# Optimization experiments

Measured on AMD Instinct MI355X. Metric: run time of the kernel, lower is better.

The kernel has to match this reference:

```python
import jax, jax.numpy as jnp
import numpy as np

B, C, H, W = 8, 4, 384, 384


def setup_inputs() -> dict:
    key = jax.random.key(0)
    k1, k2 = jax.random.split(key)
    outputs = jax.random.normal(k1, (B, C, H, W), dtype=jnp.float32)
    targets = jax.random.randint(k2, (B, H, W), 0, C)  # every class present w.h.p.
    return {"outputs": outputs, "targets": targets}


def _edt(is_zero):
    """Exact 2D Euclidean distance transform, batched.

    is_zero: bool [B,C,H,W], True at 'feature' pixels (distance 0 there).
    Returns float32 [B,C,H,W] distance to nearest True pixel.
    Separable exact algorithm (Meijster/Felzenszwalb-Huttenlocher style):
      phase 1: 1D distance along H via forward+backward scans;
      phase 2: dt^2(x,y) = min_j g(x,j)^2 + (y-j)^2 via a scan over y.
    """
    b, c, h, w = is_zero.shape
    BIG = jnp.float32(h + w)  # finite sentinel (exceeds any true distance)

    def pass1(carry, z):
        d = jnp.where(z, jnp.float32(0.0), jnp.minimum(carry + 1.0, BIG))
        return d, d

    init = jnp.full((b, c, w), BIG, jnp.float32)
    zt = jnp.moveaxis(is_zero, 2, 0)  # [H,B,C,W]
    _, fwd = jax.lax.scan(pass1, init, zt)
    _, bwd = jax.lax.scan(pass1, init, zt[::-1])
    g = jnp.minimum(fwd, bwd[::-1])          # [H,B,C,W] vertical 1D distances
    g2 = jnp.moveaxis(g * g, 0, 2)           # [B,C,H,W]

    j = jnp.arange(w, dtype=jnp.float32)     # candidate columns

    def pass2(_, y):
        # min over j of g(x,j)^2 + (y-j)^2  -> [B,C,H]
        return 0, jnp.min(g2 + (y - j) ** 2, axis=-1)

    _, dt2 = jax.lax.scan(pass2, 0, j)       # [W,B,C,H]
    return jnp.sqrt(jnp.moveaxis(dt2, 0, 3))  # [B,C,H,W]


def reference(outputs, targets):
    num_classes = outputs.shape[1]
    # one-hot: true_hot[b,c,h,w] = (targets[b,h,w] == c)
    true_hot = targets[:, None, :, :] == jnp.arange(num_classes)[None, :, None, None]
    dt = _edt(true_hot)                                  # 0 at class pixels
    dmax = jnp.max(dt, axis=(2, 3), keepdims=True)       # per (b,c) slice max
    dist_map = jnp.where(true_hot, -dmax, dt)            # factor = -1
    # weight=None -> ones(C); weight_matrix/weight.sum() == 1/C
    loss = jax.nn.softmax(outputs, axis=1) * dist_map / jnp.float32(num_classes)
    return jnp.mean(loss)
```

## Files before the change

kernel.cpp:

```cpp
#include <hip/hip_runtime.h>

#define B 8
#define C 4
#define H 384
#define W 384
#define HW (H * W)
#define CHW (C * H * W)
#define NTOT (B * CHW)
#define BIG2 589824
#define TPI 144
#define NBLK (B * TPI)
#define PSTR 12
#define LOG2E 1.44269504088896340736f

__device__ __forceinline__ int nearest2(unsigned long long m, int lx, int shl) {
    unsigned long long right = m >> lx;
    int dR = right ? (int)__builtin_ctzll(right) : 999;
    unsigned long long leftb = m << shl;
    int dL = leftb ? (int)__builtin_clzll(leftb) : 999;
    int d = min(dR, dL);
    return d * d;
}

__device__ __attribute__((noinline))
int ring_fallback(const int* __restrict__ tg, int xa, int ya, int c, int best) {
    for (int d = 17; d * d < best; ++d) {
        int xlo = xa - d, xhi = xa + d, ylo = ya - d, yhi = ya + d;
        for (int xx = max(xlo, 0); xx <= min(xhi, W - 1); ++xx) {
            int ddx = xx - xa;
            int bb = ddx * ddx + d * d;
            if (bb < best) {
                if (ylo >= 0 && tg[ylo * W + xx] == c) best = bb;
                if (yhi < H && tg[yhi * W + xx] == c) best = min(best, bb);
            }
        }
        for (int yy = max(ylo + 1, 0); yy <= min(yhi - 1, H - 1); ++yy) {
            int ddy = yy - ya;
            int bb = ddy * ddy + d * d;
            if (bb < best) {
                if (xlo >= 0 && tg[yy * W + xlo] == c) best = bb;
                if (xhi < W && tg[yy * W + xhi] == c) best = min(best, bb);
            }
        }
    }
    return best;
}

__global__ __launch_bounds__(256)
void dist_loss_kernel(const float* __restrict__ outputs,
                      const int* __restrict__ targets,
                      float* __restrict__ parts) {
    __shared__ unsigned long long rowsm[64][4];
    __shared__ unsigned long long big[32 * 18];
    __shared__ float sred[4][9];

    int bid = blockIdx.x;
    int bx = bid % 12, by = (bid / 12) % 12, b = bid / TPI;
    int x0 = bx * 32, y0 = by * 32;
    int tid = threadIdx.x, lane = tid & 63, wv = tid >> 6;
    const int* tg = targets + b * HW;

    bool edge = (bx == 0) | (bx == 11) | (by == 0) | (by == 11);
    if (!edge) {
        const int* tp = tg + (y0 - 16 + wv) * W + (x0 - 16 + lane);
        for (int i = 0; i < 16; ++i) {
            int r = i * 4 + wv;
            int tv = tp[i * 4 * W];
            unsigned long long m0 = __ballot(tv == 0);
            unsigned long long m1 = __ballot(tv == 1);
            unsigned long long m2 = __ballot(tv == 2);
            unsigned long long m3 = __ballot(tv == 3);
            if (lane == 0) {
                rowsm[r][0] = m0; rowsm[r][1] = m1;
                rowsm[r][2] = m2; rowsm[r][3] = m3;
            }
        }
    } else {
        for (int i = 0; i < 16; ++i) {
            int r = i * 4 + wv;
            int ya = y0 - 16 + r, xa = x0 - 16 + lane;
            bool valid = (ya >= 0) & (ya < H) & (xa >= 0) & (xa < W);
            int yc = min(max(ya, 0), H - 1), xc = min(max(xa, 0), W - 1);
            int tv = tg[yc * W + xc];
            unsigned long long m0 = __ballot(valid && tv == 0);
            unsigned long long m1 = __ballot(valid && tv == 1);
            unsigned long long m2 = __ballot(valid && tv == 2);
            unsigned long long m3 = __ballot(valid && tv == 3);
            if (lane == 0) {
                rowsm[r][0] = m0; rowsm[r][1] = m1;
                rowsm[r][2] = m2; rowsm[r][3] = m3;
            }
        }
    }
    __syncthreads();

    #pragma unroll
    for (int q = 0; q < 2; ++q) {
        int idx = tid + 256 * q;
        int yy = idx >> 4, c = (idx >> 2) & 3, lvl = idx & 3;
        unsigned long long v = (lvl == 0)
            ? rowsm[16 + yy][c]
            : (rowsm[16 + yy - lvl][c] | rowsm[16 + yy + lvl][c]);
        big[yy * 18 + c * 4 + lvl] = v;
    }
    __syncthreads();

    int x = tid & 31, yb = tid >> 5;
    int lx = x + 16, shl = 63 - lx;

    float red[9];
    #pragma unroll
    for (int j = 0; j < 9; ++j) red[j] = 0.0f;

    #pragma unroll
    for (int k = 0; k < 4; ++k) {
        int y = yb + 8 * k;
        int xa = x0 + x, ya = y0 + y, ly = y + 16;

        const float* ob = outputs + (size_t)b * CHW + ya * W + xa;
        float e0 = exp2f(ob[0] * LOG2E);
        float e1 = exp2f(ob[HW] * LOG2E);
        float e2 = exp2f(ob[2 * HW] * LOG2E);
        float e3 = exp2f(ob[3 * HW] * LOG2E);
        float inv = 1.0f / (e0 + e1 + e2 + e3);
        float pr[4] = {e0 * inv, e1 * inv, e2 * inv, e3 * inv};

        #pragma unroll
        for (int c = 0; c < 4; ++c) {
            const ulonglong2* pp = (const ulonglong2*)&big[y * 18 + c * 4];
            ulonglong2 v0 = pp[0], v1 = pp[1];
            int n0 = nearest2(v0.x, lx, shl);
            int n1 = nearest2(v0.y, lx, shl) + 1;
            int n2 = nearest2(v1.x, lx, shl) + 4;
            int n3 = nearest2(v1.y, lx, shl) + 9;
            int best = min(min(n0, n1), min(n2, n3));
            if (best > 16) {
                for (int dy = 4; dy <= 16 && dy * dy < best; ++dy) {
                    unsigned long long m = rowsm[ly + dy][c] | rowsm[ly - dy][c];
                    if (m) best = min(best, dy * dy + nearest2(m, lx, shl));
                }
                if (best > 289) {
                    best = min(best, BIG2);
                    best = ring_fallback(tg, xa, ya, c, best);
                }
            }
            float dt = sqrtf((float)best);
            red[0] += pr[c] * dt;
            if ((v0.x >> lx) & 1ull) red[1 + c] += pr[c];
            red[5 + c] = fmaxf(red[5 + c], dt);
        }
    }

    #pragma unroll
    for (int off = 32; off > 0; off >>= 1) {
        #pragma unroll
        for (int j = 0; j < 5; ++j) red[j] += __shfl_down(red[j], off);
        #pragma unroll
        for (int j = 5; j < 9; ++j) red[j] = fmaxf(red[j], __shfl_down(red[j], off));
    }
    if (lane == 0) {
        #pragma unroll
        for (int j = 0; j < 9; ++j) sred[wv][j] = red[j];
    }
    __syncthreads();
    if (tid == 0) {
        float o[9];
        #pragma unroll
        for (int j = 0; j < 9; ++j) o[j] = sred[0][j];
        #pragma unroll
        for (int w = 1; w < 4; ++w) {
            #pragma unroll
            for (int j = 0; j < 5; ++j) o[j] += sred[w][j];
            #pragma unroll
            for (int j = 5; j < 9; ++j) o[j] = fmaxf(o[j], sred[w][j]);
        }
        #pragma unroll
        for (int j = 0; j < 9; ++j) parts[bid * PSTR + j] = o[j];
    }
}

__global__ __launch_bounds__(256)
void finalize(const float* __restrict__ parts, float* __restrict__ out) {
    __shared__ double asum[4];
    __shared__ double Tsh[32];
    __shared__ float Msh[32];
    int tid = threadIdx.x, lane = tid & 63, wv = tid >> 6;

    double a = 0.0;
    for (int i = tid; i < NBLK; i += 256) a += (double)parts[i * PSTR];
    #pragma unroll
    for (int off = 32; off > 0; off >>= 1) a += __shfl_down(a, off);
    if (lane == 0) asum[wv] = a;

    for (int k = 0; k < 8; ++k) {
        int s = wv * 8 + k;
        int b = s >> 2, c = s & 3;
        double ts = 0.0;
        float ms = 0.0f;
        for (int i = lane; i < TPI; i += 64) {
            int blk = b * TPI + i;
            ts += (double)parts[blk * PSTR + 1 + c];
            ms = fmaxf(ms, parts[blk * PSTR + 5 + c]);
        }
        #pragma unroll
        for (int off = 32; off > 0; off >>= 1) {
            ts += __shfl_down(ts, off);
            ms = fmaxf(ms, __shfl_down(ms, off));
        }
        if (lane == 0) { Tsh[s] = ts; Msh[s] = ms; }
    }
    __syncthreads();
    if (tid == 0) {
        double A = asum[0] + asum[1] + asum[2] + asum[3];
        double st = 0.0;
        for (int s = 0; s < 32; ++s) st += (double)Msh[s] * Tsh[s];
        out[0] = (float)((A - st) / ((double)C * (double)NTOT));
    }
}

extern "C" void kernel_launch(void* const* d_in, const int* in_sizes, int n_in,
                              void* d_out, int out_size, void* d_ws, size_t ws_size,
                              hipStream_t stream) {
    const float* outputs = (const float*)d_in[0];
    const int* targets = (const int*)d_in[1];
    float* out = (float*)d_out;
    float* parts = (float*)d_ws;

    dist_loss_kernel<<<NBLK, 256, 0, stream>>>(outputs, targets, parts);
    finalize<<<1, 256, 0, stream>>>(parts, out);
}
```

Baseline: 98.72 us.

## Process four adjacent pixels per thread with float4 loads and 32-bit bit scans

Each thread now handles four horizontally adjacent pixels in one row, not one pixel in each of four rows. Logits are read as float4 vectors, and the row bitmasks are shifted once per class so each pixel's nearest-neighbour search uses 32-bit ctz/clz instead of 64-bit ones. The per-block partials layout moves from a 12-float stride to a structure-of-arrays layout, so the finalize kernel's reads are coalesced. In exchange, register pressure rises and the slow-path branches now diverge within a thread's four pixels.

```diff
diff --git a/kernel.cpp b/kernel.cpp
--- a/kernel.cpp
+++ b/kernel.cpp
@@ -10,7 +10,6 @@
 #define BIG2 589824
 #define TPI 144
 #define NBLK (B * TPI)
-#define PSTR 12
 #define LOG2E 1.44269504088896340736f
 
 __device__ __forceinline__ int nearest2(unsigned long long m, int lx, int shl) {
@@ -20,6 +19,13 @@
     int dL = leftb ? (int)__builtin_clzll(leftb) : 999;
     int d = min(dR, dL);
     return d * d;
+}
+
+__device__ __forceinline__ int scan32(unsigned int right, unsigned int left, int add) {
+    int dR = right ? __builtin_ctz(right) : 999;
+    int dL = left ? __builtin_clz(left) : 999;
+    int d = min(dR, dL);
+    return d * d + add;
 }
 
 __device__ __attribute__((noinline))
@@ -105,48 +111,74 @@
     }
     __syncthreads();
 
-    int x = tid & 31, yb = tid >> 5;
-    int lx = x + 16, shl = 63 - lx;
+    int xq = (tid & 7) * 4;
+    int y = tid >> 3;
+    int ya = y0 + y, ly = y + 16;
 
     float red[9];
     #pragma unroll
     for (int j = 0; j < 9; ++j) red[j] = 0.0f;
 
-    #pragma unroll
-    for (int k = 0; k < 4; ++k) {
-        int y = yb + 8 * k;
-        int xa = x0 + x, ya = y0 + y, ly = y + 16;
-
-        const float* ob = outputs + (size_t)b * CHW + ya * W + xa;
-        float e0 = exp2f(ob[0] * LOG2E);
-        float e1 = exp2f(ob[HW] * LOG2E);
-        float e2 = exp2f(ob[2 * HW] * LOG2E);
-        float e3 = exp2f(ob[3 * HW] * LOG2E);
-        float inv = 1.0f / (e0 + e1 + e2 + e3);
-        float pr[4] = {e0 * inv, e1 * inv, e2 * inv, e3 * inv};
-
+    float pr[4][4];
+    {
+        const float* ob = outputs + (size_t)b * CHW + (size_t)ya * W + (x0 + xq);
+        float4 f[4];
+        f[0] = *(const float4*)ob;
+        f[1] = *(const float4*)(ob + HW);
+        f[2] = *(const float4*)(ob + 2 * HW);
+        f[3] = *(const float4*)(ob + 3 * HW);
         #pragma unroll
         for (int c = 0; c < 4; ++c) {
-            const ulonglong2* pp = (const ulonglong2*)&big[y * 18 + c * 4];
-            ulonglong2 v0 = pp[0], v1 = pp[1];
-            int n0 = nearest2(v0.x, lx, shl);
-            int n1 = nearest2(v0.y, lx, shl) + 1;
-            int n2 = nearest2(v1.x, lx, shl) + 4;
-            int n3 = nearest2(v1.y, lx, shl) + 9;
-            int best = min(min(n0, n1), min(n2, n3));
+            const float* fc = (const float*)&f[c];
+            #pragma unroll
+            for (int p = 0; p < 4; ++p) pr[c][p] = exp2f(fc[p] * LOG2E);
+        }
+        #pragma unroll
+        for (int p = 0; p < 4; ++p) {
+            float inv = 1.0f / (pr[0][p] + pr[1][p] + pr[2][p] + pr[3][p]);
+            #pragma unroll
+            for (int c = 0; c < 4; ++c) pr[c][p] *= inv;
+        }
+    }
+
+    #pragma unroll
+    for (int c = 0; c < 4; ++c) {
+        const ulonglong2* pp = (const ulonglong2*)&big[y * 18 + c * 4];
+        ulonglong2 va = pp[0], vb = pp[1];
+        unsigned long long r0 = va.x >> xq;
+        unsigned long long r1 = va.y >> xq;
+        unsigned long long r2 = vb.x >> xq;
+        unsigned long long r3 = vb.y >> xq;
+        unsigned int l0 = (unsigned int)r0, l1 = (unsigned int)r1;
+        unsigned int l2 = (unsigned int)r2, l3 = (unsigned int)r3;
+        #pragma unroll
+        for (int p = 0; p < 4; ++p) {
+            unsigned int w0r = (unsigned int)(r0 >> (16 + p));
+            unsigned int w1r = (unsigned int)(r1 >> (16 + p));
+            unsigned int w2r = (unsigned int)(r2 >> (16 + p));
+            unsigned int w3r = (unsigned int)(r3 >> (16 + p));
+            unsigned int w0l = l0 << (15 - p);
+            unsigned int w1l = l1 << (15 - p);
+            unsigned int w2l = l2 << (15 - p);
+            unsigned int w3l = l3 << (15 - p);
+            int best = scan32(w0r, w0l, 0);
+            best = min(best, scan32(w1r, w1l, 1));
+            best = min(best, scan32(w2r, w2l, 4));
+            best = min(best, scan32(w3r, w3l, 9));
             if (best > 16) {
+                int lx = 16 + xq + p, shl = 63 - lx;
                 for (int dy = 4; dy <= 16 && dy * dy < best; ++dy) {
-                    unsigned long long m = rowsm[ly + dy][c] | rowsm[ly - dy][c];
-                    if (m) best = min(best, dy * dy + nearest2(m, lx, shl));
+                    unsigned long long mm = rowsm[ly + dy][c] | rowsm[ly - dy][c];
+                    if (mm) best = min(best, dy * dy + nearest2(mm, lx, shl));
                 }
                 if (best > 289) {
                     best = min(best, BIG2);
-                    best = ring_fallback(tg, xa, ya, c, best);
+                    best = ring_fallback(tg, x0 + xq + p, ya, c, best);
                 }
             }
             float dt = sqrtf((float)best);
-            red[0] += pr[c] * dt;
-            if ((v0.x >> lx) & 1ull) red[1 + c] += pr[c];
+            red[0] += pr[c][p] * dt;
+            if (w0r & 1u) red[1 + c] += pr[c][p];
             red[5 + c] = fmaxf(red[5 + c], dt);
         }
     }
@@ -175,7 +207,7 @@
             for (int j = 5; j < 9; ++j) o[j] = fmaxf(o[j], sred[w][j]);
         }
         #pragma unroll
-        for (int j = 0; j < 9; ++j) parts[bid * PSTR + j] = o[j];
+        for (int j = 0; j < 9; ++j) parts[j * NBLK + bid] = o[j];
     }
 }
 
@@ -187,7 +219,7 @@
     int tid = threadIdx.x, lane = tid & 63, wv = tid >> 6;
 
     double a = 0.0;
-    for (int i = tid; i < NBLK; i += 256) a += (double)parts[i * PSTR];
+    for (int i = tid; i < NBLK; i += 256) a += (double)parts[i];
     #pragma unroll
     for (int off = 32; off > 0; off >>= 1) a += __shfl_down(a, off);
     if (lane == 0) asum[wv] = a;
@@ -199,8 +231,8 @@
         float ms = 0.0f;
         for (int i = lane; i < TPI; i += 64) {
             int blk = b * TPI + i;
-            ts += (double)parts[blk * PSTR + 1 + c];
-            ms = fmaxf(ms, parts[blk * PSTR + 5 + c]);
+            ts += (double)parts[(1 + c) * NBLK + blk];
+            ms = fmaxf(ms, parts[(5 + c) * NBLK + blk]);
         }
         #pragma unroll
         for (int off = 32; off > 0; off >>= 1) {
```

Measured after the change: 93.97 us. 1.05x faster.

## Precompute per-row class bitmasks in a separate kernel and shrink tiles

Applied to the files above, without the earlier changes.

Adds a build_masks kernel that converts targets into per-row, per-class 64-bit ballot masks once. The main kernel then builds its 40-row halo window from these masks instead of re-reading and ballotting 64 target rows per block. Tiles go from 32x32 to 32x8 pixels, so the grid has 4x more blocks with one pixel per thread. The partials array moves to a structure-of-arrays layout for coalesced reads in finalize. The costs are an extra kernel launch, a global round trip for the masks, and the halo overhead of 40 rows per 8 output rows.

```diff
diff --git a/kernel.cpp b/kernel.cpp
--- a/kernel.cpp
+++ b/kernel.cpp
@@ -8,9 +8,9 @@
 #define CHW (C * H * W)
 #define NTOT (B * CHW)
 #define BIG2 589824
-#define TPI 144
+#define TPI 576
 #define NBLK (B * TPI)
-#define PSTR 12
+#define NSEG (B * H * 6)
 #define LOG2E 1.44269504088896340736f
 
 __device__ __forceinline__ int nearest2(unsigned long long m, int lx, int shl) {
@@ -47,57 +47,60 @@
 }
 
 __global__ __launch_bounds__(256)
+void build_masks(const int* __restrict__ targets,
+                 unsigned long long* __restrict__ masks) {
+    int wv = threadIdx.x >> 6, lane = threadIdx.x & 63;
+    int seg = blockIdx.x * 4 + wv;
+    if (seg >= NSEG) return;
+    int wd = seg % 6, rem = seg / 6;
+    int tv = targets[rem * W + wd * 64 + lane];
+    unsigned long long m0 = __ballot(tv == 0);
+    unsigned long long m1 = __ballot(tv == 1);
+    unsigned long long m2 = __ballot(tv == 2);
+    unsigned long long m3 = __ballot(tv == 3);
+    if (lane == 0) {
+        unsigned long long* dst = masks + (size_t)rem * 24 + wd;
+        dst[0]  = m0;
+        dst[6]  = m1;
+        dst[12] = m2;
+        dst[18] = m3;
+    }
+}
+
+__global__ __launch_bounds__(256)
 void dist_loss_kernel(const float* __restrict__ outputs,
                       const int* __restrict__ targets,
+                      const unsigned long long* __restrict__ masks,
                       float* __restrict__ parts) {
-    __shared__ unsigned long long rowsm[64][4];
-    __shared__ unsigned long long big[32 * 18];
+    __shared__ unsigned long long rowsm[40][4];
+    __shared__ unsigned long long big[8 * 18];
     __shared__ float sred[4][9];
 
     int bid = blockIdx.x;
-    int bx = bid % 12, by = (bid / 12) % 12, b = bid / TPI;
-    int x0 = bx * 32, y0 = by * 32;
+    int bx = bid % 12, by = (bid / 12) % 48, b = bid / TPI;
+    int x0 = bx * 32, y0 = by * 8;
     int tid = threadIdx.x, lane = tid & 63, wv = tid >> 6;
     const int* tg = targets + b * HW;
 
-    bool edge = (bx == 0) | (bx == 11) | (by == 0) | (by == 11);
-    if (!edge) {
-        const int* tp = tg + (y0 - 16 + wv) * W + (x0 - 16 + lane);
-        for (int i = 0; i < 16; ++i) {
-            int r = i * 4 + wv;
-            int tv = tp[i * 4 * W];
-            unsigned long long m0 = __ballot(tv == 0);
-            unsigned long long m1 = __ballot(tv == 1);
-            unsigned long long m2 = __ballot(tv == 2);
-            unsigned long long m3 = __ballot(tv == 3);
-            if (lane == 0) {
-                rowsm[r][0] = m0; rowsm[r][1] = m1;
-                rowsm[r][2] = m2; rowsm[r][3] = m3;
-            }
-        }
-    } else {
-        for (int i = 0; i < 16; ++i) {
-            int r = i * 4 + wv;
-            int ya = y0 - 16 + r, xa = x0 - 16 + lane;
-            bool valid = (ya >= 0) & (ya < H) & (xa >= 0) & (xa < W);
-            int yc = min(max(ya, 0), H - 1), xc = min(max(xa, 0), W - 1);
-            int tv = tg[yc * W + xc];
-            unsigned long long m0 = __ballot(valid && tv == 0);
-            unsigned long long m1 = __ballot(valid && tv == 1);
-            unsigned long long m2 = __ballot(valid && tv == 2);
-            unsigned long long m3 = __ballot(valid && tv == 3);
-            if (lane == 0) {
-                rowsm[r][0] = m0; rowsm[r][1] = m1;
-                rowsm[r][2] = m2; rowsm[r][3] = m3;
-            }
-        }
-    }
-    __syncthreads();
-
-    #pragma unroll
-    for (int q = 0; q < 2; ++q) {
-        int idx = tid + 256 * q;
-        int yy = idx >> 4, c = (idx >> 2) & 3, lvl = idx & 3;
+    if (tid < 160) {
+        int r = tid >> 2, cc = tid & 3;
+        int yaS = y0 - 16 + r;
+        unsigned long long wmask = 0ull;
+        if (yaS >= 0 && yaS < H) {
+            const unsigned long long* mrow =
+                masks + ((size_t)(b * H + yaS)) * 24 + cc * 6;
+            int bitpos = x0 - 16;
+            int iw = bitpos >> 6, sh = bitpos & 63;
+            unsigned long long lo = (iw >= 0) ? mrow[iw] : 0ull;
+            unsigned long long hi = (iw + 1 < 6) ? mrow[iw + 1] : 0ull;
+            wmask = (lo >> sh) | (hi << (64 - sh));
+        }
+        rowsm[r][cc] = wmask;
+    }
+    __syncthreads();
+
+    if (tid < 128) {
+        int yy = tid >> 4, c = (tid >> 2) & 3, lvl = tid & 3;
         unsigned long long v = (lvl == 0)
             ? rowsm[16 + yy][c]
             : (rowsm[16 + yy - lvl][c] | rowsm[16 + yy + lvl][c]);
@@ -105,50 +108,45 @@
     }
     __syncthreads();
 
-    int x = tid & 31, yb = tid >> 5;
+    int x = tid & 31, y = tid >> 5;
+    int xa = x0 + x, ya = y0 + y, ly = y + 16;
     int lx = x + 16, shl = 63 - lx;
 
     float red[9];
     #pragma unroll
     for (int j = 0; j < 9; ++j) red[j] = 0.0f;
 
-    #pragma unroll
-    for (int k = 0; k < 4; ++k) {
-        int y = yb + 8 * k;
-        int xa = x0 + x, ya = y0 + y, ly = y + 16;
-
-        const float* ob = outputs + (size_t)b * CHW + ya * W + xa;
-        float e0 = exp2f(ob[0] * LOG2E);
-        float e1 = exp2f(ob[HW] * LOG2E);
-        float e2 = exp2f(ob[2 * HW] * LOG2E);
-        float e3 = exp2f(ob[3 * HW] * LOG2E);
-        float inv = 1.0f / (e0 + e1 + e2 + e3);
-        float pr[4] = {e0 * inv, e1 * inv, e2 * inv, e3 * inv};
-
-        #pragma unroll
-        for (int c = 0; c < 4; ++c) {
-            const ulonglong2* pp = (const ulonglong2*)&big[y * 18 + c * 4];
-            ulonglong2 v0 = pp[0], v1 = pp[1];
-            int n0 = nearest2(v0.x, lx, shl);
-            int n1 = nearest2(v0.y, lx, shl) + 1;
-            int n2 = nearest2(v1.x, lx, shl) + 4;
-            int n3 = nearest2(v1.y, lx, shl) + 9;
-            int best = min(min(n0, n1), min(n2, n3));
-            if (best > 16) {
-                for (int dy = 4; dy <= 16 && dy * dy < best; ++dy) {
-                    unsigned long long m = rowsm[ly + dy][c] | rowsm[ly - dy][c];
-                    if (m) best = min(best, dy * dy + nearest2(m, lx, shl));
-                }
-                if (best > 289) {
-                    best = min(best, BIG2);
-                    best = ring_fallback(tg, xa, ya, c, best);
-                }
-            }
-            float dt = sqrtf((float)best);
-            red[0] += pr[c] * dt;
-            if ((v0.x >> lx) & 1ull) red[1 + c] += pr[c];
-            red[5 + c] = fmaxf(red[5 + c], dt);
-        }
+    const float* ob = outputs + (size_t)b * CHW + (size_t)ya * W + xa;
+    float e0 = exp2f(ob[0] * LOG2E);
+    float e1 = exp2f(ob[HW] * LOG2E);
+    float e2 = exp2f(ob[2 * HW] * LOG2E);
+    float e3 = exp2f(ob[3 * HW] * LOG2E);
+    float inv = 1.0f / (e0 + e1 + e2 + e3);
+    float pr[4] = {e0 * inv, e1 * inv, e2 * inv, e3 * inv};
+
+    #pragma unroll
+    for (int c = 0; c < 4; ++c) {
+        const ulonglong2* pp = (const ulonglong2*)&big[y * 18 + c * 4];
+        ulonglong2 v0 = pp[0], v1 = pp[1];
+        int n0 = nearest2(v0.x, lx, shl);
+        int n1 = nearest2(v0.y, lx, shl) + 1;
+        int n2 = nearest2(v1.x, lx, shl) + 4;
+        int n3 = nearest2(v1.y, lx, shl) + 9;
+        int best = min(min(n0, n1), min(n2, n3));
+        if (best > 16) {
+            for (int dy = 4; dy <= 16 && dy * dy < best; ++dy) {
+                unsigned long long m = rowsm[ly + dy][c] | rowsm[ly - dy][c];
+                if (m) best = min(best, dy * dy + nearest2(m, lx, shl));
+            }
+            if (best > 289) {
+                best = min(best, BIG2);
+                best = ring_fallback(tg, xa, ya, c, best);
+            }
+        }
+        float dt = sqrtf((float)best);
+        red[0] += pr[c] * dt;
+        if ((v0.x >> lx) & 1ull) red[1 + c] += pr[c];
+        red[5 + c] = fmaxf(red[5 + c], dt);
     }
 
     #pragma unroll
@@ -175,7 +173,7 @@
             for (int j = 5; j < 9; ++j) o[j] = fmaxf(o[j], sred[w][j]);
         }
         #pragma unroll
-        for (int j = 0; j < 9; ++j) parts[bid * PSTR + j] = o[j];
+        for (int j = 0; j < 9; ++j) parts[j * NBLK + bid] = o[j];
     }
 }
 
@@ -187,20 +185,20 @@
     int tid = threadIdx.x, lane = tid & 63, wv = tid >> 6;
 
     double a = 0.0;
-    for (int i = tid; i < NBLK; i += 256) a += (double)parts[i * PSTR];
+    for (int i = tid; i < NBLK; i += 256) a += (double)parts[i];
     #pragma unroll
     for (int off = 32; off > 0; off >>= 1) a += __shfl_down(a, off);
     if (lane == 0) asum[wv] = a;
 
     for (int k = 0; k < 8; ++k) {
         int s = wv * 8 + k;
-        int b = s >> 2, c = s & 3;
+        int bb = s >> 2, cc = s & 3;
         double ts = 0.0;
         float ms = 0.0f;
         for (int i = lane; i < TPI; i += 64) {
-            int blk = b * TPI + i;
-            ts += (double)parts[blk * PSTR + 1 + c];
-            ms = fmaxf(ms, parts[blk * PSTR + 5 + c]);
+            int blk = bb * TPI + i;
+            ts += (double)parts[(1 + cc) * NBLK + blk];
+            ms = fmaxf(ms, parts[(5 + cc) * NBLK + blk]);
         }
         #pragma unroll
         for (int off = 32; off > 0; off >>= 1) {
@@ -225,7 +223,10 @@
     const int* targets = (const int*)d_in[1];
     float* out = (float*)d_out;
     float* parts = (float*)d_ws;
-
-    dist_loss_kernel<<<NBLK, 256, 0, stream>>>(outputs, targets, parts);
+    unsigned long long* masks =
+        (unsigned long long*)((char*)d_ws + 256 * 1024);
+
+    build_masks<<<NSEG / 4, 256, 0, stream>>>(targets, masks);
+    dist_loss_kernel<<<NBLK, 256, 0, stream>>>(outputs, targets, masks, parts);
     finalize<<<1, 256, 0, stream>>>(parts, out);
 }
```

Measured after the change: 116.1 us. 17.6% more time.
